# Optimization experiments

Hardware: AMD Instinct MI355X
Metric: run time of the kernel (lower is better)

## Reference

```python
import jax, jax.numpy as jnp
import numpy as np
from jax import lax

# Kernel / geometry constants matching init_kwargs
KZ, KX, KY = 9, 15, 15          # PSF support
STRIDE = (1, 1, 1)              # scale = (zscale, xscale, yscale)
Z_PAD = (KZ - 1 + 1) // 2       # 4
X_PAD = (KX - 1 + 1) // 2       # 7
Y_PAD = (KY - 1 + 1) // 2       # 7


def _dist(n):
    # |idx - n//2|, matching _distance_from_center
    return jnp.abs(jnp.arange(n, dtype=jnp.float32) - n // 2)


def gen_psf(bet_xy, bet_z, alpha):
    b = bet_xy.shape[0]
    zd = _dist(KZ)                                  # [KZ]
    xd = _dist(KX)
    yd = _dist(KY)
    # gen_distance_plane: dp[i, j] = xd[j]^2 + yd[i]^2  (shape [KY, KX])
    dp = yd[:, None] ** 2 + xd[None, :] ** 2
    # gen_2dnorm: [b, KY, KX]
    bxy = bet_xy[:, None, None]
    lat = jnp.exp(-dp[None] / (2.0 * bxy ** 2)) / (2.0 * jnp.pi * bxy ** 2)
    # gen_1dnorm: [b, KZ]
    bz = bet_z[:, None]
    ax = jnp.exp(-(zd[None] ** 2) / (2.0 * bz ** 2)) / (jnp.sqrt(2.0 * jnp.pi) * bz)
    # psf = exp(log(lateral) + log(axial)) == lateral * axial  -> [b, 1, KZ, KY, KX]
    psf = lat[:, None, None, :, :] * ax[:, None, :, None, None]
    # double_exp mode
    psf = 1.0 - jnp.exp(-alpha[:, None, None, None, None] * psf)
    return psf / jnp.sum(psf)


def reference(x, bet_xy, bet_z, alpha):
    # x: [B, 1, Z, X, Y]; original computes dense conv3d giving [B, B, ...] and
    # keeps only the diagonal _x[b, b]. That is mathematically a per-sample
    # (grouped) convolution, implemented here without the O(B) redundancy.
    psf = gen_psf(bet_xy, bet_z, alpha)             # [B, 1, KZ, KY, KX]
    B = x.shape[0]
    xin = jnp.transpose(x, (1, 0, 2, 3, 4))         # [1, B, Z, X, Y]
    out = lax.conv_general_dilated(
        xin, psf,
        window_strides=STRIDE,
        padding=[(Z_PAD, Z_PAD), (X_PAD, X_PAD), (Y_PAD, Y_PAD)],
        dimension_numbers=("NCDHW", "OIDHW", "NCDHW"),
        feature_group_count=B,
    )                                               # [1, B, Z', X', Y']
    return jnp.transpose(out, (1, 0, 2, 3, 4))      # [B, 1, Z', X', Y']


def setup_inputs() -> dict:
    key = jax.random.key(0)
    k1, k2, k3, k4 = jax.random.split(key, 4)
    B = 4
    x = jax.random.normal(k1, (B, 1, 32, 192, 192), dtype=jnp.float32)
    bet_xy = 1.0 + 2.0 * jax.random.uniform(k2, (B,), dtype=jnp.float32)   # in [1, 3)
    bet_z = 1.0 + 2.0 * jax.random.uniform(k3, (B,), dtype=jnp.float32)    # in [1, 3)
    alpha = 1.0 + 9.0 * jax.random.uniform(k4, (B,), dtype=jnp.float32)    # in [1, 10)
    return {"x": x, "bet_xy": bet_xy, "bet_z": bet_z, "alpha": alpha}
```

## Files before the change

### kernel.cpp

```cpp
#include <hip/hip_runtime.h>
#include <math.h>

#define B_ 4
#define D_ 32
#define H_ 192
#define W_ 192
#define HW_ (H_ * W_)

#define NT 5

#define TW 48
#define TH 12
#define NTHR 256
#define ZCHUNK 16
#define NP (ZCHUNK + 8)

#define XT_H 26
#define XT_COLS 62
#define XT_W 72
#define XT_CELLS (XT_H * XT_COLS)
#define NSEC 7

#define R_S 48
#define R_H 26

#define XT_SZ (XT_H * XT_W)
#define SMEM_WORDS (2 * XT_SZ + 2 * NT * R_H * R_S)

#define NTAPS (B_ * 9 * 15 * 15)

__device__ inline float4 f4fma(float c, float4 a, float4 d) {
    d.x = fmaf(c, a.x, d.x); d.y = fmaf(c, a.y, d.y);
    d.z = fmaf(c, a.z, d.z); d.w = fmaf(c, a.w, d.w);
    return d;
}
__device__ inline float4 f4add(float4 a, float4 b) {
    a.x += b.x; a.y += b.y; a.z += b.z; a.w += b.w; return a;
}
__device__ inline float rfl(float x) {
    return __int_as_float(__builtin_amdgcn_readfirstlane(__float_as_int(x)));
}

__global__ __launch_bounds__(NTHR)
void conv_kernel(const float* __restrict__ x,
                 const float* __restrict__ bet_xy,
                 const float* __restrict__ bet_z,
                 const float* __restrict__ alpha,
                 float* __restrict__ out) {
    __shared__ __align__(16) float smem[SMEM_WORDS];
    float* xtb = smem;
    float* Rb  = smem + 2 * XT_SZ;
    float* red = smem;
    float* ct  = smem + 512;

    const int t  = threadIdx.x;
    const int w0 = blockIdx.x * TW;
    const int h0 = blockIdx.y * TH;
    const int bz = blockIdx.z;
    const int b  = bz & 3;
    const int z0 = (bz >> 2) * ZCHUNK;
    const float INV = 0.3989422804014327f;

    float local = 0.f;
#pragma unroll
    for (int s = 0; s < 32; ++s) {
        int idx = t + s * NTHR;
        if (idx < NTAPS) {
            int bb = idx / 2025;
            int r  = idx % 2025;
            int dz = r / 225;
            int r2 = r % 225;
            int dh = r2 / 15;
            int dw = r2 % 15;
            float bxy = bet_xy[bb], bzv = bet_z[bb], al = alpha[bb];
            float zd = (float)(dz - 4), hd = (float)(dh - 7), wd = (float)(dw - 7);
            float az = expf(-zd * zd / (2.f * bzv * bzv)) * (INV / bzv);
            float gh = expf(-hd * hd / (2.f * bxy * bxy)) * (INV / bxy);
            float gw = expf(-wd * wd / (2.f * bxy * bxy)) * (INV / bxy);
            local += 1.f - expf(-al * az * gh * gw);
        }
    }
    red[t] = local;
    __syncthreads();
    for (int s = 128; s > 0; s >>= 1) {
        if (t < s) red[t] += red[t + s];
        __syncthreads();
    }
    const float S = red[0];
    __syncthreads();

    if (t < NT * 13) {
        int n = t / 13;
        int k = t % 13;
        float bxy = bet_xy[b], bzv = bet_z[b], al = alpha[b];
        if (k < 8) {
            float d = (float)k;
            float g = expf(-d * d / (2.f * bxy * bxy)) * (INV / bxy);
            float p = g;
            for (int q = 0; q < n; ++q) p *= g;
            ct[n * 16 + k] = p;
        } else {
            float d = (float)(k - 8);
            float az = expf(-d * d / (2.f * bzv * bzv)) * (INV / bzv);
            float base = al * az;
            float p = base;
            for (int q = 0; q < n; ++q) p *= base;
            const float facs[NT] = {1.f, 2.f, 6.f, 24.f, 120.f};
            float sign = (n & 1) ? -1.f : 1.f;
            ct[n * 16 + k] = sign * p / (facs[n] * S);
        }
    }
    __syncthreads();

    float cg_[NT][8], cz_[NT][5];
#pragma unroll
    for (int n = 0; n < NT; ++n) {
#pragma unroll
        for (int k = 0; k < 8; ++k) cg_[n][k] = rfl(ct[n * 16 + k]);
#pragma unroll
        for (int k = 0; k < 5; ++k) cz_[n][k] = rfl(ct[n * 16 + 8 + k]);
    }
    __syncthreads();

    const float* xb = x + (size_t)b * (D_ * HW_);
    int goff[NSEC], loff[NSEC];
#pragma unroll
    for (int k = 0; k < NSEC; ++k) {
        int i = t + k * NTHR;
        int r = i / XT_COLS, c = i - r * XT_COLS;
        int gh = h0 + r - 7, gw = w0 + c - 7;
        bool ok = (i < XT_CELLS) && gh >= 0 && gh < H_ && gw >= 0 && gw < W_;
        goff[k] = ok ? (gh * W_ + gw) : -1;
        loff[k] = (i < XT_CELLS) ? (r * XT_W + c) : (XT_SZ - 1);
    }
    {
        int zi0 = z0 - 4;
        if (zi0 >= 0) {
#pragma unroll
            for (int k = 0; k < NSEC; ++k) {
                float v = 0.f;
                if (goff[k] >= 0) v = xb[(size_t)zi0 * HW_ + goff[k]];
                xtb[loff[k]] = v;
            }
        }
    }

    const int i0r = t / 12,  i0c = t - 12 * i0r;
    const int i1  = t + 56;
    const int i1r = i1 / 12, i1c = i1 - 12 * i1r;
    const bool sec1 = (t >= 200);
    const int wb0 = i0r * XT_W + 4 * i0c, rw0 = i0r * R_S + 4 * i0c;
    const int wb1 = i1r * XT_W + 4 * i1c, rw1 = i1r * R_S + 4 * i1c;
    const bool hact = (t < TH * 12);
    const int ro = t / 12, cgh = t - 12 * ro;
    const int hb = ro * R_S + 4 * cgh;

    float4 acc[9];
#pragma unroll
    for (int k = 0; k < 9; ++k) acc[k] = make_float4(0.f, 0.f, 0.f, 0.f);

#pragma unroll 1
    for (int p = 0; p <= NP; ++p) {
        __syncthreads();

        const int zi = z0 - 4 + p;
        const bool do_w  = (p < NP) && (zi >= 0) && (zi < D_);
        const int  zn    = zi + 1;
        const bool pvalid = (p + 1 < NP) && (zn >= 0) && (zn < D_);

        float pv[NSEC];
        if (pvalid) {
            const float* xp = xb + (size_t)zn * HW_;
#pragma unroll
            for (int k = 0; k < NSEC; ++k) pv[k] = (goff[k] >= 0) ? xp[goff[k]] : 0.f;
        }

        if (do_w) {
            const float* xt = xtb + (p & 1) * XT_SZ;
            float* Rw = Rb + (p & 1) * (NT * R_H * R_S);
#pragma unroll
            for (int sec = 0; sec < 2; ++sec) {
                if (sec == 1 && !sec1) break;
                const int wb = sec ? wb1 : wb0;
                const int rw = sec ? rw1 : rw0;
                float win[20];
                {
                    const float4* p4 = (const float4*)&xt[wb];
#pragma unroll
                    for (int q = 0; q < 5; ++q) {
                        float4 a = p4[q];
                        win[4 * q] = a.x; win[4 * q + 1] = a.y;
                        win[4 * q + 2] = a.z; win[4 * q + 3] = a.w;
                    }
                }
                float cj[4], sp[4][7];
#pragma unroll
                for (int j = 0; j < 4; ++j) {
                    cj[j] = win[j + 7];
#pragma unroll
                    for (int k = 1; k <= 7; ++k) sp[j][k - 1] = win[j + 7 - k] + win[j + 7 + k];
                }
#pragma unroll
                for (int n = 0; n < NT; ++n) {
                    float4 a;
                    a.x = cg_[n][0] * cj[0]; a.y = cg_[n][0] * cj[1];
                    a.z = cg_[n][0] * cj[2]; a.w = cg_[n][0] * cj[3];
#pragma unroll
                    for (int k = 1; k <= 7; ++k) {
                        float c = cg_[n][k];
                        a.x = fmaf(c, sp[0][k - 1], a.x);
                        a.y = fmaf(c, sp[1][k - 1], a.y);
                        a.z = fmaf(c, sp[2][k - 1], a.z);
                        a.w = fmaf(c, sp[3][k - 1], a.w);
                    }
                    *(float4*)&Rw[n * (R_H * R_S) + rw] = a;
                }
            }
        }

        if (p >= 1) {
            const int ziq = zi - 1;
            if (hact) {
                if (ziq >= 0 && ziq < D_) {
                    const float* Rr = Rb + ((p - 1) & 1) * (NT * R_H * R_S);
#pragma unroll
                    for (int n = 0; n < NT; ++n) {
                        const float* R1 = Rr + n * (R_H * R_S);
                        float4 rv[15];
#pragma unroll
                        for (int dh = 0; dh < 15; ++dh)
                            rv[dh] = *(const float4*)&R1[hb + dh * R_S];
                        float4 q;
                        q.x = cg_[n][0] * rv[7].x; q.y = cg_[n][0] * rv[7].y;
                        q.z = cg_[n][0] * rv[7].z; q.w = cg_[n][0] * rv[7].w;
#pragma unroll
                        for (int k = 1; k <= 7; ++k)
                            q = f4fma(cg_[n][k], f4add(rv[7 - k], rv[7 + k]), q);
                        acc[4] = f4fma(cz_[n][0], q, acc[4]);
#pragma unroll
                        for (int j = 1; j <= 4; ++j) {
                            float cz = cz_[n][j];
                            acc[4 + j] = f4fma(cz, q, acc[4 + j]);
                            acc[4 - j] = f4fma(cz, q, acc[4 - j]);
                        }
                    }
                }
                if (p - 1 >= 8) {
                    int z = z0 + (p - 1 - 8);
                    size_t o = ((size_t)(b * D_ + z) * H_ + (h0 + ro)) * W_ + (w0 + 4 * cgh);
                    *(float4*)&out[o] = acc[0];
                }
#pragma unroll
                for (int k = 0; k < 8; ++k) acc[k] = acc[k + 1];
                acc[8] = make_float4(0.f, 0.f, 0.f, 0.f);
            }
        }

        if (pvalid) {
            float* xn = xtb + ((p + 1) & 1) * XT_SZ;
#pragma unroll
            for (int k = 0; k < NSEC; ++k) xn[loff[k]] = pv[k];
        }
    }
}

extern "C" void kernel_launch(void* const* d_in, const int* in_sizes, int n_in,
                              void* d_out, int out_size, void* d_ws, size_t ws_size,
                              hipStream_t stream) {
    const float* x      = (const float*)d_in[0];
    const float* bet_xy = (const float*)d_in[1];
    const float* bet_z  = (const float*)d_in[2];
    const float* alpha  = (const float*)d_in[3];
    float* out = (float*)d_out;

    hipLaunchKernelGGL(conv_kernel, dim3(W_ / TW, H_ / TH, B_ * (D_ / ZCHUNK)),
                       dim3(NTHR), 0, stream, x, bet_xy, bet_z, alpha, out);
}
```

Baseline: 157.0 us.

## Transpose intermediate row-pass buffer to column-major for contiguous vertical pass reads

Stores the W-direction filtered intermediate in a column-major (transposed) shared buffer with stride 28, so the H-direction pass reads 20 contiguous values per thread via five float4 loads instead of fifteen strided float4 loads. Each thread in the vertical pass now computes four consecutive rows of one column, and output writes become four scalar stores strided by the row width instead of one float4 store. This trades scattered scalar LDS writes in the first pass and uncoalesced-vector global stores for fewer LDS reads in the second pass.

```diff
diff --git a/kernel.cpp b/kernel.cpp
--- a/kernel.cpp
+++ b/kernel.cpp
@@ -21,11 +21,12 @@
 #define XT_CELLS (XT_H * XT_COLS)
 #define NSEC 7
 
-#define R_S 48
-#define R_H 26
+#define R_TS 28
+#define CTERM (TW * R_TS)
+#define RBUF (NT * CTERM)
 
 #define XT_SZ (XT_H * XT_W)
-#define SMEM_WORDS (2 * XT_SZ + 2 * NT * R_H * R_S)
+#define SMEM_WORDS (2 * XT_SZ + 2 * RBUF)
 
 #define NTAPS (B_ * 9 * 15 * 15)
 
@@ -33,9 +34,6 @@
     d.x = fmaf(c, a.x, d.x); d.y = fmaf(c, a.y, d.y);
     d.z = fmaf(c, a.z, d.z); d.w = fmaf(c, a.w, d.w);
     return d;
-}
-__device__ inline float4 f4add(float4 a, float4 b) {
-    a.x += b.x; a.y += b.y; a.z += b.z; a.w += b.w; return a;
 }
 __device__ inline float rfl(float x) {
     return __int_as_float(__builtin_amdgcn_readfirstlane(__float_as_int(x)));
@@ -145,15 +143,18 @@
         }
     }
 
-    const int i0r = t / 12,  i0c = t - 12 * i0r;
+    const int i0r = t % 26,  i0c = t / 26;
     const int i1  = t + 56;
-    const int i1r = i1 / 12, i1c = i1 - 12 * i1r;
+    const int i1r = i1 % 26, i1c = i1 / 26;
     const bool sec1 = (t >= 200);
-    const int wb0 = i0r * XT_W + 4 * i0c, rw0 = i0r * R_S + 4 * i0c;
-    const int wb1 = i1r * XT_W + 4 * i1c, rw1 = i1r * R_S + 4 * i1c;
-    const bool hact = (t < TH * 12);
-    const int ro = t / 12, cgh = t - 12 * ro;
-    const int hb = ro * R_S + 4 * cgh;
+    const int wb0 = i0r * XT_W + 4 * i0c;
+    const int rw0 = (4 * i0c) * R_TS + i0r;
+    const int wb1 = i1r * XT_W + 4 * i1c;
+    const int rw1 = (4 * i1c) * R_TS + i1r;
+    const bool hact = (t < TW * 3);
+    const int hc = t % TW, hq = t / TW;
+    const int r0 = 4 * hq;
+    const int hb = hc * R_TS + r0;
 
     float4 acc[9];
 #pragma unroll
@@ -177,7 +178,7 @@
 
         if (do_w) {
             const float* xt = xtb + (p & 1) * XT_SZ;
-            float* Rw = Rb + (p & 1) * (NT * R_H * R_S);
+            float* Rw = Rb + (p & 1) * RBUF;
 #pragma unroll
             for (int sec = 0; sec < 2; ++sec) {
                 if (sec == 1 && !sec1) break;
@@ -202,58 +203,71 @@
                 }
 #pragma unroll
                 for (int n = 0; n < NT; ++n) {
-                    float4 a;
-                    a.x = cg_[n][0] * cj[0]; a.y = cg_[n][0] * cj[1];
-                    a.z = cg_[n][0] * cj[2]; a.w = cg_[n][0] * cj[3];
+                    float a0 = cg_[n][0] * cj[0];
+                    float a1 = cg_[n][0] * cj[1];
+                    float a2 = cg_[n][0] * cj[2];
+                    float a3 = cg_[n][0] * cj[3];
 #pragma unroll
                     for (int k = 1; k <= 7; ++k) {
                         float c = cg_[n][k];
-                        a.x = fmaf(c, sp[0][k - 1], a.x);
-                        a.y = fmaf(c, sp[1][k - 1], a.y);
-                        a.z = fmaf(c, sp[2][k - 1], a.z);
-                        a.w = fmaf(c, sp[3][k - 1], a.w);
-                    }
-                    *(float4*)&Rw[n * (R_H * R_S) + rw] = a;
-                }
-            }
-        }
-
-        if (p >= 1) {
+                        a0 = fmaf(c, sp[0][k - 1], a0);
+                        a1 = fmaf(c, sp[1][k - 1], a1);
+                        a2 = fmaf(c, sp[2][k - 1], a2);
+                        a3 = fmaf(c, sp[3][k - 1], a3);
+                    }
+                    float* q = Rw + n * CTERM + rw;
+                    q[0] = a0; q[R_TS] = a1; q[2 * R_TS] = a2; q[3 * R_TS] = a3;
+                }
+            }
+        }
+
+        if (p >= 1 && hact) {
             const int ziq = zi - 1;
-            if (hact) {
-                if (ziq >= 0 && ziq < D_) {
-                    const float* Rr = Rb + ((p - 1) & 1) * (NT * R_H * R_S);
-#pragma unroll
-                    for (int n = 0; n < NT; ++n) {
-                        const float* R1 = Rr + n * (R_H * R_S);
-                        float4 rv[15];
-#pragma unroll
-                        for (int dh = 0; dh < 15; ++dh)
-                            rv[dh] = *(const float4*)&R1[hb + dh * R_S];
-                        float4 q;
-                        q.x = cg_[n][0] * rv[7].x; q.y = cg_[n][0] * rv[7].y;
-                        q.z = cg_[n][0] * rv[7].z; q.w = cg_[n][0] * rv[7].w;
-#pragma unroll
-                        for (int k = 1; k <= 7; ++k)
-                            q = f4fma(cg_[n][k], f4add(rv[7 - k], rv[7 + k]), q);
-                        acc[4] = f4fma(cz_[n][0], q, acc[4]);
-#pragma unroll
-                        for (int j = 1; j <= 4; ++j) {
-                            float cz = cz_[n][j];
-                            acc[4 + j] = f4fma(cz, q, acc[4 + j]);
-                            acc[4 - j] = f4fma(cz, q, acc[4 - j]);
-                        }
-                    }
-                }
-                if (p - 1 >= 8) {
-                    int z = z0 + (p - 1 - 8);
-                    size_t o = ((size_t)(b * D_ + z) * H_ + (h0 + ro)) * W_ + (w0 + 4 * cgh);
-                    *(float4*)&out[o] = acc[0];
-                }
-#pragma unroll
-                for (int k = 0; k < 8; ++k) acc[k] = acc[k + 1];
-                acc[8] = make_float4(0.f, 0.f, 0.f, 0.f);
-            }
+            if (ziq >= 0 && ziq < D_) {
+                const float* Rr = Rb + ((p - 1) & 1) * RBUF;
+#pragma unroll
+                for (int n = 0; n < NT; ++n) {
+                    const float* R1 = Rr + n * CTERM + hb;
+                    float v[20];
+#pragma unroll
+                    for (int k = 0; k < 5; ++k) {
+                        float4 a = *(const float4*)&R1[4 * k];
+                        v[4 * k] = a.x; v[4 * k + 1] = a.y;
+                        v[4 * k + 2] = a.z; v[4 * k + 3] = a.w;
+                    }
+                    float4 q;
+                    q.x = cg_[n][0] * v[7];
+                    q.y = cg_[n][0] * v[8];
+                    q.z = cg_[n][0] * v[9];
+                    q.w = cg_[n][0] * v[10];
+#pragma unroll
+                    for (int m = 1; m <= 7; ++m) {
+                        float c = cg_[n][m];
+                        q.x = fmaf(c, v[7 - m]  + v[7 + m],  q.x);
+                        q.y = fmaf(c, v[8 - m]  + v[8 + m],  q.y);
+                        q.z = fmaf(c, v[9 - m]  + v[9 + m],  q.z);
+                        q.w = fmaf(c, v[10 - m] + v[10 + m], q.w);
+                    }
+                    acc[4] = f4fma(cz_[n][0], q, acc[4]);
+#pragma unroll
+                    for (int j = 1; j <= 4; ++j) {
+                        float cz = cz_[n][j];
+                        acc[4 + j] = f4fma(cz, q, acc[4 + j]);
+                        acc[4 - j] = f4fma(cz, q, acc[4 - j]);
+                    }
+                }
+            }
+            if (p - 1 >= 8) {
+                int z = z0 + (p - 1 - 8);
+                size_t o = ((size_t)(b * D_ + z) * H_ + (h0 + r0)) * W_ + (w0 + hc);
+                out[o]          = acc[0].x;
+                out[o + W_]     = acc[0].y;
+                out[o + 2 * W_] = acc[0].z;
+                out[o + 3 * W_] = acc[0].w;
+            }
+#pragma unroll
+            for (int k = 0; k < 8; ++k) acc[k] = acc[k + 1];
+            acc[8] = make_float4(0.f, 0.f, 0.f, 0.f);
         }
 
         if (pvalid) {
```

Result: slower. 168.7 us (+7.5%).

## Split H-conv terms across waves with 2-row register blocking and single R buffer

Applied to the files above, without the earlier changes.

Restructures the vertical (H) pass so each thread computes two output rows from 16 loaded rows, which reuses shared-memory loads. The five separable terms are split between two wave groups that are reduced through a small shared scratch buffer. R is single-buffered with an extra barrier, and the x tile pitch is shrunk, which reduces LDS use so two blocks fit per CU under launch_bounds(256,2). The cost is an extra __syncthreads per iteration, more registers for the doubled accumulators, and a one-step-delayed cross-wave reduction.

```diff
diff --git a/kernel.cpp b/kernel.cpp
--- a/kernel.cpp
+++ b/kernel.cpp
@@ -17,15 +17,20 @@
 
 #define XT_H 26
 #define XT_COLS 62
-#define XT_W 72
+#define XT_W 68
 #define XT_CELLS (XT_H * XT_COLS)
+#define XT_SZ (XT_H * XT_W)
 #define NSEC 7
 
 #define R_S 48
 #define R_H 26
-
-#define XT_SZ (XT_H * XT_W)
-#define SMEM_WORDS (2 * XT_SZ + 2 * NT * R_H * R_S)
+#define CTERM (R_H * R_S)
+#define RWORDS (NT * CTERM)
+
+#define NITEM 72
+#define SCR_WORDS (2 * NITEM * 8)
+
+#define SMEM_WORDS (RWORDS + 2 * XT_SZ + SCR_WORDS)
 
 #define NTAPS (B_ * 9 * 15 * 15)
 
@@ -41,15 +46,50 @@
     return __int_as_float(__builtin_amdgcn_readfirstlane(__float_as_int(x)));
 }
 
-__global__ __launch_bounds__(NTHR)
+template <int N0, int N1>
+__device__ __forceinline__ void hconv(const float* __restrict__ Rr, int hb,
+                                      const float cg_[NT][8], const float cz_[NT][5],
+                                      float4 acc[9][2]) {
+#pragma unroll
+    for (int n = N0; n < N1; ++n) {
+        const float* R1 = Rr + n * CTERM + hb;
+        float4 v[16];
+#pragma unroll
+        for (int j = 0; j < 16; ++j) v[j] = *(const float4*)&R1[j * R_S];
+        float4 q0, q1;
+        q0.x = cg_[n][0] * v[7].x;  q0.y = cg_[n][0] * v[7].y;
+        q0.z = cg_[n][0] * v[7].z;  q0.w = cg_[n][0] * v[7].w;
+        q1.x = cg_[n][0] * v[8].x;  q1.y = cg_[n][0] * v[8].y;
+        q1.z = cg_[n][0] * v[8].z;  q1.w = cg_[n][0] * v[8].w;
+#pragma unroll
+        for (int m = 1; m <= 7; ++m) {
+            float c = cg_[n][m];
+            q0 = f4fma(c, f4add(v[7 - m], v[7 + m]), q0);
+            q1 = f4fma(c, f4add(v[8 - m], v[8 + m]), q1);
+        }
+        acc[4][0] = f4fma(cz_[n][0], q0, acc[4][0]);
+        acc[4][1] = f4fma(cz_[n][0], q1, acc[4][1]);
+#pragma unroll
+        for (int j = 1; j <= 4; ++j) {
+            float cz = cz_[n][j];
+            acc[4 + j][0] = f4fma(cz, q0, acc[4 + j][0]);
+            acc[4 + j][1] = f4fma(cz, q1, acc[4 + j][1]);
+            acc[4 - j][0] = f4fma(cz, q0, acc[4 - j][0]);
+            acc[4 - j][1] = f4fma(cz, q1, acc[4 - j][1]);
+        }
+    }
+}
+
+__global__ __launch_bounds__(NTHR, 2)
 void conv_kernel(const float* __restrict__ x,
                  const float* __restrict__ bet_xy,
                  const float* __restrict__ bet_z,
                  const float* __restrict__ alpha,
                  float* __restrict__ out) {
     __shared__ __align__(16) float smem[SMEM_WORDS];
-    float* xtb = smem;
-    float* Rb  = smem + 2 * XT_SZ;
+    float* Rm  = smem;
+    float* xtb = smem + RWORDS;
+    float* scr = smem + RWORDS + 2 * XT_SZ;
     float* red = smem;
     float* ct  = smem + 512;
 
@@ -151,21 +191,29 @@
     const bool sec1 = (t >= 200);
     const int wb0 = i0r * XT_W + 4 * i0c, rw0 = i0r * R_S + 4 * i0c;
     const int wb1 = i1r * XT_W + 4 * i1c, rw1 = i1r * R_S + 4 * i1c;
-    const bool hact = (t < TH * 12);
-    const int ro = t / 12, cgh = t - 12 * ro;
-    const int hb = ro * R_S + 4 * cgh;
-
-    float4 acc[9];
-#pragma unroll
-    for (int k = 0; k < 9; ++k) acc[k] = make_float4(0.f, 0.f, 0.f, 0.f);
+    const int wv = t >> 6, ln = t & 63;
+    const bool hA = (wv == 0) || (wv == 2 && ln < 8);
+    const bool hB = (wv == 1) || (wv == 3 && ln < 8);
+    const bool hact = hA || hB;
+    const int hitem = (wv <= 1) ? ln : (64 + ln);
+    const int hq  = hitem / 12, hcg = hitem - 12 * hq;
+    const int hb  = (2 * hq) * R_S + 4 * hcg;
+
+    float4 acc[9][2];
+#pragma unroll
+    for (int k = 0; k < 9; ++k) {
+        acc[k][0] = make_float4(0.f, 0.f, 0.f, 0.f);
+        acc[k][1] = make_float4(0.f, 0.f, 0.f, 0.f);
+    }
+    float4 pend0 = make_float4(0.f, 0.f, 0.f, 0.f);
+    float4 pend1 = make_float4(0.f, 0.f, 0.f, 0.f);
 
 #pragma unroll 1
-    for (int p = 0; p <= NP; ++p) {
+    for (int p = 0; p <= NP + 1; ++p) {
         __syncthreads();
 
         const int zi = z0 - 4 + p;
-        const bool do_w  = (p < NP) && (zi >= 0) && (zi < D_);
-        const int  zn    = zi + 1;
+        const int zn = zi + 1;
         const bool pvalid = (p + 1 < NP) && (zn >= 0) && (zn < D_);
 
         float pv[NSEC];
@@ -175,9 +223,42 @@
             for (int k = 0; k < NSEC; ++k) pv[k] = (goff[k] >= 0) ? xp[goff[k]] : 0.f;
         }
 
-        if (do_w) {
+        if (hact && p >= 1) {
+            const int ziq = z0 - 5 + p;
+            if (p <= NP && ziq >= 0 && ziq < D_) {
+                if (hA) hconv<0, 3>(Rm, hb, cg_, cz_, acc);
+                else    hconv<3, 5>(Rm, hb, cg_, cz_, acc);
+            }
+            if (p >= 10 && hA) {
+                const float* sc = &scr[(((p - 1) & 1) * NITEM + hitem) * 8];
+                float4 s0 = *(const float4*)&sc[0];
+                float4 s1 = *(const float4*)&sc[4];
+                float4 o0 = f4add(pend0, s0);
+                float4 o1 = f4add(pend1, s1);
+                int z = z0 + p - 10;
+                size_t o = ((size_t)(b * D_ + z) * H_ + (h0 + 2 * hq)) * W_ + (w0 + 4 * hcg);
+                *(float4*)&out[o] = o0;
+                *(float4*)&out[o + W_] = o1;
+            }
+            float4 lv0 = acc[0][0], lv1 = acc[0][1];
+#pragma unroll
+            for (int k = 0; k < 8; ++k) { acc[k][0] = acc[k + 1][0]; acc[k][1] = acc[k + 1][1]; }
+            acc[8][0] = make_float4(0.f, 0.f, 0.f, 0.f);
+            acc[8][1] = make_float4(0.f, 0.f, 0.f, 0.f);
+            if (p >= 9) {
+                if (hA) { pend0 = lv0; pend1 = lv1; }
+                else {
+                    float* sc = &scr[((p & 1) * NITEM + hitem) * 8];
+                    *(float4*)&sc[0] = lv0;
+                    *(float4*)&sc[4] = lv1;
+                }
+            }
+        }
+
+        __syncthreads();
+
+        if (p < NP && zi >= 0 && zi < D_) {
             const float* xt = xtb + (p & 1) * XT_SZ;
-            float* Rw = Rb + (p & 1) * (NT * R_H * R_S);
 #pragma unroll
             for (int sec = 0; sec < 2; ++sec) {
                 if (sec == 1 && !sec1) break;
@@ -213,49 +294,10 @@
                         a.z = fmaf(c, sp[2][k - 1], a.z);
                         a.w = fmaf(c, sp[3][k - 1], a.w);
                     }
-                    *(float4*)&Rw[n * (R_H * R_S) + rw] = a;
+                    *(float4*)&Rm[n * CTERM + rw] = a;
                 }
             }
         }
-
-        if (p >= 1) {
-            const int ziq = zi - 1;
-            if (hact) {
-                if (ziq >= 0 && ziq < D_) {
-                    const float* Rr = Rb + ((p - 1) & 1) * (NT * R_H * R_S);
-#pragma unroll
-                    for (int n = 0; n < NT; ++n) {
-                        const float* R1 = Rr + n * (R_H * R_S);
-                        float4 rv[15];
-#pragma unroll
-                        for (int dh = 0; dh < 15; ++dh)
-                            rv[dh] = *(const float4*)&R1[hb + dh * R_S];
-                        float4 q;
-                        q.x = cg_[n][0] * rv[7].x; q.y = cg_[n][0] * rv[7].y;
-                        q.z = cg_[n][0] * rv[7].z; q.w = cg_[n][0] * rv[7].w;
-#pragma unroll
-                        for (int k = 1; k <= 7; ++k)
-                            q = f4fma(cg_[n][k], f4add(rv[7 - k], rv[7 + k]), q);
-                        acc[4] = f4fma(cz_[n][0], q, acc[4]);
-#pragma unroll
-                        for (int j = 1; j <= 4; ++j) {
-                            float cz = cz_[n][j];
-                            acc[4 + j] = f4fma(cz, q, acc[4 + j]);
-                            acc[4 - j] = f4fma(cz, q, acc[4 - j]);
-                        }
-                    }
-                }
-                if (p - 1 >= 8) {
-                    int z = z0 + (p - 1 - 8);
-                    size_t o = ((size_t)(b * D_ + z) * H_ + (h0 + ro)) * W_ + (w0 + 4 * cgh);
-                    *(float4*)&out[o] = acc[0];
-                }
-#pragma unroll
-                for (int k = 0; k < 8; ++k) acc[k] = acc[k + 1];
-                acc[8] = make_float4(0.f, 0.f, 0.f, 0.f);
-            }
-        }
-
         if (pvalid) {
             float* xn = xtb + ((p + 1) & 1) * XT_SZ;
 #pragma unroll
```

Result: slower. 210.7 us (+34.2%).
